# Performance work log

Measured on AMD Instinct MI355X. Metric: run time of the kernel, lower is better.

Reference implementation:

```python
import jax, jax.numpy as jnp
import numpy as np

HEAD_DIM = 32
N_HEADS = 8
Q_DIM = 128
FF_DIM = 4 * Q_DIM
EPS = 1e-5


def layernorm(x, gamma, beta):
    mu = jnp.mean(x, axis=-1, keepdims=True)
    var = jnp.var(x, axis=-1, keepdims=True)
    return (x - mu) * jax.lax.rsqrt(var + EPS) * gamma + beta


def setup_inputs() -> dict:
    key = jax.random.key(0)
    ks = jax.random.split(key, 20)
    S, B = 1024, 16
    sc_in = 1.0 / np.sqrt(Q_DIM)
    sc_hd = 1.0 / np.sqrt(N_HEADS * HEAD_DIM)
    sc_ff = 1.0 / np.sqrt(FF_DIM)
    return {
        "sequence": jax.random.normal(ks[0], (S, B, Q_DIM), jnp.float32),
        # per-head Q/K/V projections, stacked over heads: [H, Q_dim, head_dim]
        "Wq": jax.random.uniform(ks[1], (N_HEADS, Q_DIM, HEAD_DIM), jnp.float32, -sc_in, sc_in),
        "bq": jax.random.uniform(ks[2], (N_HEADS, HEAD_DIM), jnp.float32, -sc_in, sc_in),
        "Wk": jax.random.uniform(ks[3], (N_HEADS, Q_DIM, HEAD_DIM), jnp.float32, -sc_in, sc_in),
        "bk": jax.random.uniform(ks[4], (N_HEADS, HEAD_DIM), jnp.float32, -sc_in, sc_in),
        "Wv": jax.random.uniform(ks[5], (N_HEADS, Q_DIM, HEAD_DIM), jnp.float32, -sc_in, sc_in),
        "bv": jax.random.uniform(ks[6], (N_HEADS, HEAD_DIM), jnp.float32, -sc_in, sc_in),
        # post_head_linear: [H*head_dim, Q_dim]
        "Wo": jax.random.uniform(ks[7], (N_HEADS * HEAD_DIM, Q_DIM), jnp.float32, -sc_hd, sc_hd),
        "bo": jax.random.uniform(ks[8], (Q_DIM,), jnp.float32, -sc_hd, sc_hd),
        # norm1 (note: original reuses norm1 for both layernorms)
        "gamma1": jnp.ones((Q_DIM,), jnp.float32),
        "beta1": jnp.zeros((Q_DIM,), jnp.float32),
        # FFN: Q_dim -> 4Q -> 4Q -> Q_dim
        "W1": jax.random.uniform(ks[9], (Q_DIM, FF_DIM), jnp.float32, -sc_in, sc_in),
        "b1": jax.random.uniform(ks[10], (FF_DIM,), jnp.float32, -sc_in, sc_in),
        "W2": jax.random.uniform(ks[11], (FF_DIM, FF_DIM), jnp.float32, -sc_ff, sc_ff),
        "b2": jax.random.uniform(ks[12], (FF_DIM,), jnp.float32, -sc_ff, sc_ff),
        "W3": jax.random.uniform(ks[13], (FF_DIM, Q_DIM), jnp.float32, -sc_ff, sc_ff),
        "b3": jax.random.uniform(ks[14], (Q_DIM,), jnp.float32, -sc_ff, sc_ff),
    }


def reference(sequence, Wq, bq, Wk, bk, Wv, bv, Wo, bo, gamma1, beta1, W1, b1, W2, b2, W3, b3):
    # sequence: [S, B, Q_dim] -> batch-first [B, S, Q_dim]
    x = jnp.transpose(sequence, (1, 0, 2))
    # batched per-head projections: [B, H, S, d]
    q = jnp.einsum('bsq,hqd->bhsd', x, Wq) + bq[None, :, None, :]
    k = jnp.einsum('bsq,hqd->bhsd', x, Wk) + bk[None, :, None, :]
    v = jnp.einsum('bsq,hqd->bhsd', x, Wv) + bv[None, :, None, :]
    scores = jnp.einsum('bhsd,bhtd->bhst', q, k) / np.sqrt(HEAD_DIM)
    attn = jax.nn.softmax(scores, axis=-1)
    o = jnp.einsum('bhst,bhtd->bhsd', attn, v)  # [B, H, S, d]
    B, H, S, d = o.shape
    o = jnp.transpose(o, (0, 2, 1, 3)).reshape(B, S, H * d)  # concat heads
    att_outs = o @ Wo + bo
    att_outs = layernorm(x + att_outs, gamma1, beta1)
    h = jax.nn.relu(att_outs @ W1 + b1)
    h = jax.nn.relu(h @ W2 + b2)
    h = h @ W3 + b3
    out = layernorm(att_outs + h, gamma1, beta1)  # original reuses norm1
    return jnp.transpose(out, (1, 0, 2))  # back to [S, B, Q_dim]
```

## Files before the change

### kernel.cpp

```cpp
#include <hip/hip_runtime.h>
#include <hip/hip_bf16.h>

#define S_LEN 1024
#define BATCH 16
#define QD 128
#define NH 8
#define HD 32
#define FF 512
#define NROWS (BATCH * S_LEN)
#define EPS 1e-5f

typedef __attribute__((ext_vector_type(4))) float f32x4;
typedef __attribute__((ext_vector_type(8))) short s16x8;
typedef __attribute__((ext_vector_type(4))) short s16x4;

__device__ __forceinline__ ushort f2bfu(float f) {
    union { float f; unsigned u; } v; v.f = f;
    unsigned r = (v.u + 0x7FFFu + ((v.u >> 16) & 1u)) >> 16;
    return (ushort)r;
}

__device__ __forceinline__ float exp2_fast(float x) {
#if __has_builtin(__builtin_amdgcn_exp2f)
    return __builtin_amdgcn_exp2f(x);
#else
    float r;
    asm("v_exp_f32 %0, %1" : "=v"(r) : "v"(x));
    return r;
#endif
}

__device__ __forceinline__ unsigned pk_bf16(float a, float b) {
    union { __hip_bfloat162 h; unsigned u; } c;
    c.h = __float22bfloat162_rn(make_float2(a, b));
    return c.u;
}

static __device__ __forceinline__ f32x4 mfma16(s16x4 a, s16x4 b, f32x4 c) {
#if __has_builtin(__builtin_amdgcn_mfma_f32_16x16x16bf16_1k)
    return __builtin_amdgcn_mfma_f32_16x16x16bf16_1k(a, b, c, 0, 0, 0);
#else
    asm volatile("v_mfma_f32_16x16x16_bf16 %0, %1, %2, %0" : "+v"(c) : "v"(a), "v"(b));
    return c;
#endif
}

static __device__ __forceinline__ f32x4 mfma32(s16x8 a, s16x8 b, f32x4 c) {
    return __builtin_amdgcn_mfma_f32_16x16x32_bf16(a, b, c, 0, 0, 0);
}

__device__ __forceinline__ void gl_lds16(const void* g, void* l) {
    __builtin_amdgcn_global_load_lds(
        (const __attribute__((address_space(1))) void*)g,
        (__attribute__((address_space(3))) void*)l, 16, 0, 0);
}

template <int K>
__device__ __forceinline__ void gemm_core(
    const ushort* __restrict__ act, const ushort* __restrict__ WTp,
    char* lds, int tok0, f32x4 acc[8]) {
    const int tid = threadIdx.x;
    const int w = tid >> 6, lane = tid & 63;
    const int qi = lane & 15, g = lane >> 4;
    const int r8 = tid >> 3;
    const int csw = (tid & 7) ^ (r8 & 7);
    const int wave_base = w * 1024;
    constexpr int NT = K / 64;

    auto STAGE = [&](int b, int ks) {
        char* buf = lds + b * 24576;
#pragma unroll
        for (int i = 0; i < 4; ++i)
            gl_lds16(WTp + (size_t)(i * 32 + r8) * K + ks + csw * 8,
                     buf + i * 4096 + wave_base);
#pragma unroll
        for (int j = 0; j < 2; ++j)
            gl_lds16(act + (size_t)(tok0 + j * 32 + r8) * K + ks + csw * 8,
                     buf + 16384 + j * 4096 + wave_base);
    };

    STAGE(0, 0);
    int cur = 0;
#pragma unroll 1
    for (int t = 0; t < NT; ++t) {
        if (t < NT - 1) {
            STAGE(cur ^ 1, (t + 1) * 64);
            asm volatile("s_waitcnt vmcnt(6)" ::: "memory");
        } else {
            asm volatile("s_waitcnt vmcnt(0)" ::: "memory");
        }
        __builtin_amdgcn_sched_barrier(0);
        __builtin_amdgcn_s_barrier();
        __builtin_amdgcn_sched_barrier(0);
        const char* A = lds + cur * 24576;
        const char* B = A + 16384;
        const int brow = w * 16 + qi;
        __builtin_amdgcn_s_setprio(1);
#pragma unroll
        for (int kk2 = 0; kk2 < 2; ++kk2) {
            s16x8 bfrag = *(const s16x8*)(B + brow * 128 +
                                          (((kk2 * 4 + g) ^ (brow & 7)) * 16));
#pragma unroll
            for (int f = 0; f < 8; ++f) {
                const int row = qi + 16 * f;
                s16x8 afrag = *(const s16x8*)(A + row * 128 +
                                              (((kk2 * 4 + g) ^ (row & 7)) * 16));
                acc[f] = mfma32(afrag, bfrag, acc[f]);
            }
        }
        __builtin_amdgcn_s_setprio(0);
        __builtin_amdgcn_sched_barrier(0);
        __builtin_amdgcn_s_barrier();
        __builtin_amdgcn_sched_barrier(0);
        cur ^= 1;
    }
}

__global__ __launch_bounds__(256) void prep_weights(
    const float* __restrict__ Wo, const float* __restrict__ W1,
    const float* __restrict__ W2, const float* __restrict__ W3,
    const float* __restrict__ Wq, const float* __restrict__ Wk,
    const float* __restrict__ Wv,
    ushort* __restrict__ WoT, ushort* __restrict__ W1T,
    ushort* __restrict__ W2T, ushort* __restrict__ W3T,
    ushort* __restrict__ WqkvT) {
    int idx = blockIdx.x * 256 + threadIdx.x;
    if (idx < 32768) {
        int n = idx >> 8, k = idx & 255;
        WoT[n * 256 + k] = f2bfu(Wo[k * 128 + n]);
    } else if (idx < 98304) {
        int i = idx - 32768; int n = i >> 7, k = i & 127;
        W1T[n * 128 + k] = f2bfu(W1[k * 512 + n]);
    } else if (idx < 360448) {
        int i = idx - 98304; int n = i >> 9, k = i & 511;
        W2T[n * 512 + k] = f2bfu(W2[k * 512 + n]);
    } else if (idx < 425984) {
        int i = idx - 360448; int n = i >> 9, k = i & 511;
        W3T[n * 512 + k] = f2bfu(W3[k * 128 + n]);
    } else {
        int i = idx - 425984;
        int n = i >> 7, k = i & 127;
        int p = n >> 8, h = (n >> 5) & 7, d = n & 31;
        const float* W = (p == 0) ? Wq : (p == 1) ? Wk : Wv;
        WqkvT[n * 128 + k] = f2bfu(W[(h * QD + k) * HD + d]);
    }
}

__global__ __launch_bounds__(256) void seq2bf(
    const float* __restrict__ seq, ushort* __restrict__ x_bf) {
    int t = blockIdx.x * 256 + threadIdx.x;
    int e4 = t * 4;
    int s = e4 >> 11, b = (e4 >> 7) & 15, c = e4 & 127;
    float4 v = *(const float4*)(seq + e4);
    ushort4 o = {f2bfu(v.x), f2bfu(v.y), f2bfu(v.z), f2bfu(v.w)};
    *(ushort4*)(x_bf + ((size_t)(b * 1024 + s)) * 128 + c) = o;
}

__global__ __launch_bounds__(256) void qkv_mfma(
    const ushort* __restrict__ x_bf, const ushort* __restrict__ WqkvT,
    const float* __restrict__ bq, const float* __restrict__ bk,
    const float* __restrict__ bv,
    ushort* __restrict__ q_bf, ushort* __restrict__ k_bf,
    ushort* __restrict__ vT) {
    __shared__ __align__(16) char lds[2 * 24576];
    const int lane = threadIdx.x & 63;
    const int w = threadIdx.x >> 6;
    const int qi = lane & 15, g = lane >> 4;
    const int tok0 = blockIdx.x * 64;
    const int tok = tok0 + w * 16 + qi;
    const int n0 = blockIdx.y * 128;

    f32x4 acc[8];
#pragma unroll
    for (int f = 0; f < 8; ++f) acc[f] = (f32x4){0.f, 0.f, 0.f, 0.f};
    gemm_core<128>(x_bf, WqkvT + (size_t)n0 * 128, lds, tok0, acc);

    const int b = tok >> 10, s = tok & 1023;
    const float SCALE = 0.25503491f;
    if (n0 < 256) {
#pragma unroll
        for (int f = 0; f < 8; ++f)
#pragma unroll
            for (int r = 0; r < 4; ++r) {
                int n = n0 + 16 * f + 4 * g + r;
                int h = (n >> 5) & 7, d = n & 31;
                q_bf[((size_t)(b * 8 + h) * 1024 + s) * 32 + d] =
                    f2bfu((acc[f][r] + bq[h * 32 + d]) * SCALE);
            }
    } else if (n0 < 512) {
#pragma unroll
        for (int f = 0; f < 8; ++f)
#pragma unroll
            for (int r = 0; r < 4; ++r) {
                int n = n0 + 16 * f + 4 * g + r;
                int h = (n >> 5) & 7, d = n & 31;
                k_bf[((size_t)(b * 8 + h) * 1024 + s) * 32 + d] =
                    f2bfu(acc[f][r] + bk[h * 32 + d]);
            }
    } else {
#pragma unroll
        for (int f = 0; f < 8; ++f)
#pragma unroll
            for (int r = 0; r < 4; ++r) {
                int n = n0 + 16 * f + 4 * g + r;
                int h = (n >> 5) & 7, d = n & 31;
                vT[((size_t)(b * 8 + h) * 32 + d) * 1024 + s] =
                    f2bfu(acc[f][r] + bv[h * 32 + d]);
            }
    }
}

__global__ __launch_bounds__(256) void attn_mfma(
    const ushort* __restrict__ qb, const ushort* __restrict__ kb,
    const ushort* __restrict__ vtb, ushort* __restrict__ o_bf) {
    __shared__ __align__(16) char lds[2][8192];
    const int tid = threadIdx.x;
    const int w = tid >> 6, lane = tid & 63;
    const int g = lane >> 4, qi = lane & 15;
    const int bid = blockIdx.x;
    const int swz = (bid & 7) * 256 + (bid >> 3);
    const int bh = swz >> 4;
    const int qtile = (swz & 15) * 4 + w;

    const ushort* Kb = kb + (size_t)bh * S_LEN * HD;
    const ushort* VTb = vtb + (size_t)bh * HD * S_LEN;
    const s16x8 qf = *(const s16x8*)(qb + ((size_t)bh * S_LEN + qtile * 16 + qi) * HD + g * 8);

    const int krow = tid >> 2;
    const int ksw = (tid & 3) ^ ((tid >> 3) & 3);
    const int vrow = tid >> 3;
    const int vsw = (tid & 7) ^ ((tid >> 4) & 7);
    const int wave_off = w * 1024;

#define STAGE(bufp, k0)                                                          \
    do {                                                                         \
        gl_lds16(Kb + (size_t)((k0) + krow) * HD + ksw * 8, (bufp) + wave_off);  \
        gl_lds16(VTb + (size_t)vrow * S_LEN + (k0) + vsw * 8,                    \
                 (bufp) + 4096 + wave_off);                                      \
    } while (0)

    f32x4 ot0 = {0.f, 0.f, 0.f, 0.f};
    f32x4 ot1 = {0.f, 0.f, 0.f, 0.f};
    float m_run = -1e30f, l_run = 0.f;
    const f32x4 zero = {0.f, 0.f, 0.f, 0.f};

    const int koff = (g ^ ((qi >> 1) & 3)) * 16;
    const int vs = (qi >> 1) & 7;

    STAGE(lds[0], 0);
    int cur = 0;
#pragma unroll 1
    for (int t = 0; t < 16; ++t) {
        if (t < 15) {
            STAGE(lds[cur ^ 1], (t + 1) * 64);
            asm volatile("s_waitcnt vmcnt(2)" ::: "memory");
        } else {
            asm volatile("s_waitcnt vmcnt(0)" ::: "memory");
        }
        __builtin_amdgcn_sched_barrier(0);
        __builtin_amdgcn_s_barrier();
        __builtin_amdgcn_sched_barrier(0);

        const char* kl = lds[cur];
        const char* vl = lds[cur] + 4096;
        s16x8 ka[4];
#pragma unroll
        for (int kt = 0; kt < 4; ++kt)
            ka[kt] = *(const s16x8*)(kl + (16 * kt + qi) * 64 + koff);
        s16x4 va[2][4];
#pragma unroll
        for (int h = 0; h < 2; ++h)
#pragma unroll
            for (int kt = 0; kt < 4; ++kt) {
                int c8 = 4 * kt + g;
                va[h][kt] = *(const s16x4*)(vl + (16 * h + qi) * 128 +
                                            (((c8 >> 1) ^ vs) * 16) + (c8 & 1) * 8);
            }

        f32x4 st[4];
        __builtin_amdgcn_s_setprio(1);
#pragma unroll
        for (int kt = 0; kt < 4; ++kt) st[kt] = mfma32(ka[kt], qf, zero);
        __builtin_amdgcn_s_setprio(0);

        float a0 = fmaxf(fmaxf(st[0][0], st[0][1]), fmaxf(st[0][2], st[0][3]));
        float a1 = fmaxf(fmaxf(st[1][0], st[1][1]), fmaxf(st[1][2], st[1][3]));
        float a2 = fmaxf(fmaxf(st[2][0], st[2][1]), fmaxf(st[2][2], st[2][3]));
        float a3 = fmaxf(fmaxf(st[3][0], st[3][1]), fmaxf(st[3][2], st[3][3]));
        float pmax = fmaxf(fmaxf(a0, a1), fmaxf(a2, a3));

        if (!__all(pmax <= m_run + 8.0f)) {
            float mt = pmax;
            mt = fmaxf(mt, __shfl_xor(mt, 16, 64));
            mt = fmaxf(mt, __shfl_xor(mt, 32, 64));
            float m_new = fmaxf(m_run, mt);
            float alpha = exp2_fast(m_run - m_new);
            l_run *= alpha;
#pragma unroll
            for (int r = 0; r < 4; ++r) { ot0[r] *= alpha; ot1[r] *= alpha; }
            m_run = m_new;
        }

        float p[4][4];
#pragma unroll
        for (int kt = 0; kt < 4; ++kt)
#pragma unroll
            for (int r = 0; r < 4; ++r) p[kt][r] = exp2_fast(st[kt][r] - m_run);
        float s0 = (p[0][0] + p[0][1]) + (p[0][2] + p[0][3]);
        float s1 = (p[1][0] + p[1][1]) + (p[1][2] + p[1][3]);
        float s2 = (p[2][0] + p[2][1]) + (p[2][2] + p[2][3]);
        float s3 = (p[3][0] + p[3][1]) + (p[3][2] + p[3][3]);
        l_run += (s0 + s1) + (s2 + s3);

        union { s16x4 v; uint2 u; } pb[4];
#pragma unroll
        for (int kt = 0; kt < 4; ++kt) {
            pb[kt].u.x = pk_bf16(p[kt][0], p[kt][1]);
            pb[kt].u.y = pk_bf16(p[kt][2], p[kt][3]);
        }
        __builtin_amdgcn_s_setprio(1);
#pragma unroll
        for (int kt = 0; kt < 4; ++kt) {
            ot0 = mfma16(va[0][kt], pb[kt].v, ot0);
            ot1 = mfma16(va[1][kt], pb[kt].v, ot1);
        }
        __builtin_amdgcn_s_setprio(0);

        __builtin_amdgcn_sched_barrier(0);
        __builtin_amdgcn_s_barrier();
        __builtin_amdgcn_sched_barrier(0);
        cur ^= 1;
    }
#undef STAGE

    l_run += __shfl_xor(l_run, 16, 64);
    l_run += __shfl_xor(l_run, 32, 64);
    const float inv_l = 1.0f / l_run;
    const int b = bh >> 3, head = bh & 7;
    const int qg = qtile * 16 + qi;
    ushort* orow = o_bf + ((size_t)(b * S_LEN + qg)) * (NH * HD) + head * HD;
    ushort4 ob0 = {f2bfu(ot0[0] * inv_l), f2bfu(ot0[1] * inv_l),
                   f2bfu(ot0[2] * inv_l), f2bfu(ot0[3] * inv_l)};
    ushort4 ob1 = {f2bfu(ot1[0] * inv_l), f2bfu(ot1[1] * inv_l),
                   f2bfu(ot1[2] * inv_l), f2bfu(ot1[3] * inv_l)};
    *(ushort4*)(orow + g * 4) = ob0;
    *(ushort4*)(orow + 16 + g * 4) = ob1;
}

__global__ __launch_bounds__(256) void wo_ln_mfma(
    const ushort* __restrict__ o_bf, const ushort* __restrict__ WoT,
    const float* __restrict__ bo, const float* __restrict__ seq,
    const float* __restrict__ gamma, const float* __restrict__ beta,
    float* __restrict__ att, ushort* __restrict__ att_bf) {
    __shared__ __align__(16) char lds[2 * 24576];
    const int lane = threadIdx.x & 63;
    const int w = threadIdx.x >> 6;
    const int qi = lane & 15, g = lane >> 4;
    const int tok0 = blockIdx.x * 64;
    const int tok = tok0 + w * 16 + qi;

    f32x4 acc[8];
#pragma unroll
    for (int f = 0; f < 8; ++f) acc[f] = (f32x4){0.f, 0.f, 0.f, 0.f};
    gemm_core<256>(o_bf, WoT, lds, tok0, acc);

    const int b = tok >> 10, s = tok & 1023;
    const float* xrow = seq + (size_t)(s * BATCH + b) * QD;
    float sum = 0.f, sumsq = 0.f;
#pragma unroll
    for (int f = 0; f < 8; ++f) {
        const int c = 16 * f + 4 * g;
        float4 bv = *(const float4*)(bo + c);
        float4 xv = *(const float4*)(xrow + c);
        acc[f][0] += bv.x + xv.x;
        acc[f][1] += bv.y + xv.y;
        acc[f][2] += bv.z + xv.z;
        acc[f][3] += bv.w + xv.w;
#pragma unroll
        for (int r = 0; r < 4; ++r) { sum += acc[f][r]; sumsq += acc[f][r] * acc[f][r]; }
    }
    sum += __shfl_xor(sum, 16, 64);
    sum += __shfl_xor(sum, 32, 64);
    sumsq += __shfl_xor(sumsq, 16, 64);
    sumsq += __shfl_xor(sumsq, 32, 64);
    const float mu = sum * (1.0f / QD);
    const float var = sumsq * (1.0f / QD) - mu * mu;
    const float rstd = rsqrtf(var + EPS);

#pragma unroll
    for (int f = 0; f < 8; ++f) {
        const int c = 16 * f + 4 * g;
        float4 gm = *(const float4*)(gamma + c);
        float4 bt = *(const float4*)(beta + c);
        float4 ov;
        ov.x = (acc[f][0] - mu) * rstd * gm.x + bt.x;
        ov.y = (acc[f][1] - mu) * rstd * gm.y + bt.y;
        ov.z = (acc[f][2] - mu) * rstd * gm.z + bt.z;
        ov.w = (acc[f][3] - mu) * rstd * gm.w + bt.w;
        *(float4*)(att + (size_t)tok * QD + c) = ov;
        ushort4 pv = {f2bfu(ov.x), f2bfu(ov.y), f2bfu(ov.z), f2bfu(ov.w)};
        *(ushort4*)(att_bf + (size_t)tok * QD + c) = pv;
    }
}

template <int K>
__global__ __launch_bounds__(256) void ffn_mfma(
    const ushort* __restrict__ act, const ushort* __restrict__ WT,
    const float* __restrict__ bias, ushort* __restrict__ out, int N) {
    __shared__ __align__(16) char lds[2 * 24576];
    const int lane = threadIdx.x & 63;
    const int w = threadIdx.x >> 6;
    const int qi = lane & 15, g = lane >> 4;
    const int tok0 = blockIdx.x * 64;
    const int tok = tok0 + w * 16 + qi;
    const int n0 = blockIdx.y * 128;

    f32x4 acc[8];
#pragma unroll
    for (int f = 0; f < 8; ++f) acc[f] = (f32x4){0.f, 0.f, 0.f, 0.f};
    gemm_core<K>(act, WT + (size_t)n0 * K, lds, tok0, acc);

#pragma unroll
    for (int f = 0; f < 8; ++f) {
        const int c = n0 + 16 * f + 4 * g;
        float4 bv = *(const float4*)(bias + c);
        ushort4 pv;
        pv.x = f2bfu(fmaxf(acc[f][0] + bv.x, 0.f));
        pv.y = f2bfu(fmaxf(acc[f][1] + bv.y, 0.f));
        pv.z = f2bfu(fmaxf(acc[f][2] + bv.z, 0.f));
        pv.w = f2bfu(fmaxf(acc[f][3] + bv.w, 0.f));
        *(ushort4*)(out + (size_t)tok * N + c) = pv;
    }
}

__global__ __launch_bounds__(256) void w3_ln_mfma(
    const ushort* __restrict__ h2, const ushort* __restrict__ W3T,
    const float* __restrict__ b3, const float* __restrict__ att,
    const float* __restrict__ gamma, const float* __restrict__ beta,
    float* __restrict__ out) {
    __shared__ __align__(16) char lds[2 * 24576];
    const int lane = threadIdx.x & 63;
    const int w = threadIdx.x >> 6;
    const int qi = lane & 15, g = lane >> 4;
    const int tok0 = blockIdx.x * 64;
    const int tok = tok0 + w * 16 + qi;

    f32x4 acc[8];
#pragma unroll
    for (int f = 0; f < 8; ++f) acc[f] = (f32x4){0.f, 0.f, 0.f, 0.f};
    gemm_core<512>(h2, W3T, lds, tok0, acc);

    float sum = 0.f, sumsq = 0.f;
#pragma unroll
    for (int f = 0; f < 8; ++f) {
        const int c = 16 * f + 4 * g;
        float4 bv = *(const float4*)(b3 + c);
        float4 xv = *(const float4*)(att + (size_t)tok * QD + c);
        acc[f][0] += bv.x + xv.x;
        acc[f][1] += bv.y + xv.y;
        acc[f][2] += bv.z + xv.z;
        acc[f][3] += bv.w + xv.w;
#pragma unroll
        for (int r = 0; r < 4; ++r) { sum += acc[f][r]; sumsq += acc[f][r] * acc[f][r]; }
    }
    sum += __shfl_xor(sum, 16, 64);
    sum += __shfl_xor(sum, 32, 64);
    sumsq += __shfl_xor(sumsq, 16, 64);
    sumsq += __shfl_xor(sumsq, 32, 64);
    const float mu = sum * (1.0f / QD);
    const float var = sumsq * (1.0f / QD) - mu * mu;
    const float rstd = rsqrtf(var + EPS);

    const int b = tok >> 10, s = tok & 1023;
    float* orow = out + (size_t)(s * BATCH + b) * QD;
#pragma unroll
    for (int f = 0; f < 8; ++f) {
        const int c = 16 * f + 4 * g;
        float4 gm = *(const float4*)(gamma + c);
        float4 bt = *(const float4*)(beta + c);
        float4 ov;
        ov.x = (acc[f][0] - mu) * rstd * gm.x + bt.x;
        ov.y = (acc[f][1] - mu) * rstd * gm.y + bt.y;
        ov.z = (acc[f][2] - mu) * rstd * gm.z + bt.z;
        ov.w = (acc[f][3] - mu) * rstd * gm.w + bt.w;
        *(float4*)(orow + c) = ov;
    }
}

extern "C" void kernel_launch(void* const* d_in, const int* in_sizes, int n_in,
                              void* d_out, int out_size, void* d_ws, size_t ws_size,
                              hipStream_t stream) {
    const float* seq = (const float*)d_in[0];
    const float* Wq = (const float*)d_in[1];
    const float* bq = (const float*)d_in[2];
    const float* Wk = (const float*)d_in[3];
    const float* bk = (const float*)d_in[4];
    const float* Wv = (const float*)d_in[5];
    const float* bv = (const float*)d_in[6];
    const float* Wo = (const float*)d_in[7];
    const float* bo = (const float*)d_in[8];
    const float* gamma = (const float*)d_in[9];
    const float* beta = (const float*)d_in[10];
    const float* W1 = (const float*)d_in[11];
    const float* b1 = (const float*)d_in[12];
    const float* W2 = (const float*)d_in[13];
    const float* b2 = (const float*)d_in[14];
    const float* W3 = (const float*)d_in[15];
    const float* b3 = (const float*)d_in[16];

    char* wsb = (char*)d_ws;
    ushort* q_bf  = (ushort*)(wsb);
    ushort* k_bf  = (ushort*)(wsb + (8ull << 20));
    ushort* vT    = (ushort*)(wsb + (16ull << 20));
    ushort* o_bf  = (ushort*)(wsb + (24ull << 20));
    float*  att   = (float*)(wsb + (32ull << 20));
    ushort* att_bf= (ushort*)(wsb + (40ull << 20));
    ushort* h1_bf = (ushort*)(wsb);
    ushort* h2_bf = (ushort*)(wsb + (16ull << 20));
    ushort* x_bf  = (ushort*)(wsb + (45ull << 20));
    ushort* WoT   = (ushort*)(wsb + (49ull << 20));
    ushort* W1T   = WoT + 32768;
    ushort* W2T   = W1T + 65536;
    ushort* W3T   = W2T + 262144;
    ushort* WqkvT = W3T + 65536;
    float* out = (float*)d_out;

    prep_weights<<<2048, 256, 0, stream>>>(Wo, W1, W2, W3, Wq, Wk, Wv,
                                           WoT, W1T, W2T, W3T, WqkvT);
    seq2bf<<<2048, 256, 0, stream>>>(seq, x_bf);
    qkv_mfma<<<dim3(NROWS / 64, 6), 256, 0, stream>>>(x_bf, WqkvT, bq, bk, bv,
                                                      q_bf, k_bf, vT);
    attn_mfma<<<(BATCH * NH) * 16, 256, 0, stream>>>(q_bf, k_bf, vT, o_bf);
    wo_ln_mfma<<<NROWS / 64, 256, 0, stream>>>(o_bf, WoT, bo, seq, gamma, beta, att, att_bf);
    ffn_mfma<QD><<<dim3(NROWS / 64, 4), 256, 0, stream>>>(att_bf, W1T, b1, h1_bf, FF);
    ffn_mfma<FF><<<dim3(NROWS / 64, 4), 256, 0, stream>>>(h1_bf, W2T, b2, h2_bf, FF);
    w3_ln_mfma<<<NROWS / 64, 256, 0, stream>>>(h2_bf, W3T, b3, att, gamma, beta, out);
}
```

Baseline: 116.6 us.

## Merge prep kernels, widen attention blocks to 8 waves, drop fp32 residual buffer

Folds the sequence-to-bf16 conversion into the weight prep kernel, removing one launch. The attention kernel now runs 512-thread blocks with 8 query tiles per block, so each K/V tile staged in LDS is shared by twice as many waves and each wave issues one load instead of two. The fp32 post-attention residual buffer is removed and the final layernorm reads the bf16 copy, cutting global traffic at some cost in residual precision.

```diff
diff --git a/kernel.cpp b/kernel.cpp
--- a/kernel.cpp
+++ b/kernel.cpp
@@ -18,6 +18,11 @@
     union { float f; unsigned u; } v; v.f = f;
     unsigned r = (v.u + 0x7FFFu + ((v.u >> 16) & 1u)) >> 16;
     return (ushort)r;
+}
+
+__device__ __forceinline__ float bf2f(ushort u) {
+    union { unsigned u; float f; } v; v.u = ((unsigned)u) << 16;
+    return v.f;
 }
 
 __device__ __forceinline__ float exp2_fast(float x) {
@@ -116,7 +121,8 @@
     }
 }
 
-__global__ __launch_bounds__(256) void prep_weights(
+__global__ __launch_bounds__(256) void prep_all(
+    const float* __restrict__ seq, ushort* __restrict__ x_bf,
     const float* __restrict__ Wo, const float* __restrict__ W1,
     const float* __restrict__ W2, const float* __restrict__ W3,
     const float* __restrict__ Wq, const float* __restrict__ Wk,
@@ -124,7 +130,16 @@
     ushort* __restrict__ WoT, ushort* __restrict__ W1T,
     ushort* __restrict__ W2T, ushort* __restrict__ W3T,
     ushort* __restrict__ WqkvT) {
-    int idx = blockIdx.x * 256 + threadIdx.x;
+    if (blockIdx.x < 2048) {
+        int t = blockIdx.x * 256 + threadIdx.x;
+        int e4 = t * 4;
+        int s = e4 >> 11, b = (e4 >> 7) & 15, c = e4 & 127;
+        float4 v = *(const float4*)(seq + e4);
+        ushort4 o = {f2bfu(v.x), f2bfu(v.y), f2bfu(v.z), f2bfu(v.w)};
+        *(ushort4*)(x_bf + ((size_t)(b * 1024 + s)) * 128 + c) = o;
+        return;
+    }
+    int idx = (blockIdx.x - 2048) * 256 + threadIdx.x;
     if (idx < 32768) {
         int n = idx >> 8, k = idx & 255;
         WoT[n * 256 + k] = f2bfu(Wo[k * 128 + n]);
@@ -146,16 +161,6 @@
     }
 }
 
-__global__ __launch_bounds__(256) void seq2bf(
-    const float* __restrict__ seq, ushort* __restrict__ x_bf) {
-    int t = blockIdx.x * 256 + threadIdx.x;
-    int e4 = t * 4;
-    int s = e4 >> 11, b = (e4 >> 7) & 15, c = e4 & 127;
-    float4 v = *(const float4*)(seq + e4);
-    ushort4 o = {f2bfu(v.x), f2bfu(v.y), f2bfu(v.z), f2bfu(v.w)};
-    *(ushort4*)(x_bf + ((size_t)(b * 1024 + s)) * 128 + c) = o;
-}
-
 __global__ __launch_bounds__(256) void qkv_mfma(
     const ushort* __restrict__ x_bf, const ushort* __restrict__ WqkvT,
     const float* __restrict__ bq, const float* __restrict__ bk,
@@ -210,7 +215,7 @@
     }
 }
 
-__global__ __launch_bounds__(256) void attn_mfma(
+__global__ __launch_bounds__(512) void attn_mfma(
     const ushort* __restrict__ qb, const ushort* __restrict__ kb,
     const ushort* __restrict__ vtb, ushort* __restrict__ o_bf) {
     __shared__ __align__(16) char lds[2][8192];
@@ -218,25 +223,28 @@
     const int w = tid >> 6, lane = tid & 63;
     const int g = lane >> 4, qi = lane & 15;
     const int bid = blockIdx.x;
-    const int swz = (bid & 7) * 256 + (bid >> 3);
-    const int bh = swz >> 4;
-    const int qtile = (swz & 15) * 4 + w;
+    const int swz = (bid & 7) * 128 + (bid >> 3);
+    const int bh = swz >> 3;
+    const int qtile = (swz & 7) * 8 + w;
 
     const ushort* Kb = kb + (size_t)bh * S_LEN * HD;
     const ushort* VTb = vtb + (size_t)bh * HD * S_LEN;
     const s16x8 qf = *(const s16x8*)(qb + ((size_t)bh * S_LEN + qtile * 16 + qi) * HD + g * 8);
 
-    const int krow = tid >> 2;
-    const int ksw = (tid & 3) ^ ((tid >> 3) & 3);
-    const int vrow = tid >> 3;
-    const int vsw = (tid & 7) ^ ((tid >> 4) & 7);
-    const int wave_off = w * 1024;
-
-#define STAGE(bufp, k0)                                                          \
-    do {                                                                         \
-        gl_lds16(Kb + (size_t)((k0) + krow) * HD + ksw * 8, (bufp) + wave_off);  \
-        gl_lds16(VTb + (size_t)vrow * S_LEN + (k0) + vsw * 8,                    \
-                 (bufp) + 4096 + wave_off);                                      \
+    const int krow = 16 * w + (lane >> 2);
+    const int ksrc = (lane & 3) ^ ((lane >> 3) & 3);
+    const int wv = w & 3;
+    const int vrow = 8 * wv + (lane >> 3);
+    const int vsrc = (lane & 7) ^ ((4 * wv + (lane >> 4)) & 7);
+
+#define STAGE(bufp, k0)                                                        \
+    do {                                                                       \
+        if (w < 4)                                                             \
+            gl_lds16(Kb + (size_t)((k0) + krow) * HD + ksrc * 8,               \
+                     (bufp) + w * 1024);                                       \
+        else                                                                   \
+            gl_lds16(VTb + (size_t)vrow * S_LEN + (k0) + vsrc * 8,             \
+                     (bufp) + 4096 + wv * 1024);                               \
     } while (0)
 
     f32x4 ot0 = {0.f, 0.f, 0.f, 0.f};
@@ -253,7 +261,7 @@
     for (int t = 0; t < 16; ++t) {
         if (t < 15) {
             STAGE(lds[cur ^ 1], (t + 1) * 64);
-            asm volatile("s_waitcnt vmcnt(2)" ::: "memory");
+            asm volatile("s_waitcnt vmcnt(1)" ::: "memory");
         } else {
             asm volatile("s_waitcnt vmcnt(0)" ::: "memory");
         }
@@ -351,7 +359,7 @@
     const ushort* __restrict__ o_bf, const ushort* __restrict__ WoT,
     const float* __restrict__ bo, const float* __restrict__ seq,
     const float* __restrict__ gamma, const float* __restrict__ beta,
-    float* __restrict__ att, ushort* __restrict__ att_bf) {
+    ushort* __restrict__ att_bf) {
     __shared__ __align__(16) char lds[2 * 24576];
     const int lane = threadIdx.x & 63;
     const int w = threadIdx.x >> 6;
@@ -392,13 +400,11 @@
         const int c = 16 * f + 4 * g;
         float4 gm = *(const float4*)(gamma + c);
         float4 bt = *(const float4*)(beta + c);
-        float4 ov;
-        ov.x = (acc[f][0] - mu) * rstd * gm.x + bt.x;
-        ov.y = (acc[f][1] - mu) * rstd * gm.y + bt.y;
-        ov.z = (acc[f][2] - mu) * rstd * gm.z + bt.z;
-        ov.w = (acc[f][3] - mu) * rstd * gm.w + bt.w;
-        *(float4*)(att + (size_t)tok * QD + c) = ov;
-        ushort4 pv = {f2bfu(ov.x), f2bfu(ov.y), f2bfu(ov.z), f2bfu(ov.w)};
+        ushort4 pv;
+        pv.x = f2bfu((acc[f][0] - mu) * rstd * gm.x + bt.x);
+        pv.y = f2bfu((acc[f][1] - mu) * rstd * gm.y + bt.y);
+        pv.z = f2bfu((acc[f][2] - mu) * rstd * gm.z + bt.z);
+        pv.w = f2bfu((acc[f][3] - mu) * rstd * gm.w + bt.w);
         *(ushort4*)(att_bf + (size_t)tok * QD + c) = pv;
     }
 }
@@ -435,7 +441,7 @@
 
 __global__ __launch_bounds__(256) void w3_ln_mfma(
     const ushort* __restrict__ h2, const ushort* __restrict__ W3T,
-    const float* __restrict__ b3, const float* __restrict__ att,
+    const float* __restrict__ b3, const ushort* __restrict__ att_bf,
     const float* __restrict__ gamma, const float* __restrict__ beta,
     float* __restrict__ out) {
     __shared__ __align__(16) char lds[2 * 24576];
@@ -455,11 +461,11 @@
     for (int f = 0; f < 8; ++f) {
         const int c = 16 * f + 4 * g;
         float4 bv = *(const float4*)(b3 + c);
-        float4 xv = *(const float4*)(att + (size_t)tok * QD + c);
-        acc[f][0] += bv.x + xv.x;
-        acc[f][1] += bv.y + xv.y;
-        acc[f][2] += bv.z + xv.z;
-        acc[f][3] += bv.w + xv.w;
+        ushort4 xv = *(const ushort4*)(att_bf + (size_t)tok * QD + c);
+        acc[f][0] += bv.x + bf2f(xv.x);
+        acc[f][1] += bv.y + bf2f(xv.y);
+        acc[f][2] += bv.z + bf2f(xv.z);
+        acc[f][3] += bv.w + bf2f(xv.w);
 #pragma unroll
         for (int r = 0; r < 4; ++r) { sum += acc[f][r]; sumsq += acc[f][r] * acc[f][r]; }
     }
@@ -513,7 +519,6 @@
     ushort* k_bf  = (ushort*)(wsb + (8ull << 20));
     ushort* vT    = (ushort*)(wsb + (16ull << 20));
     ushort* o_bf  = (ushort*)(wsb + (24ull << 20));
-    float*  att   = (float*)(wsb + (32ull << 20));
     ushort* att_bf= (ushort*)(wsb + (40ull << 20));
     ushort* h1_bf = (ushort*)(wsb);
     ushort* h2_bf = (ushort*)(wsb + (16ull << 20));
@@ -525,14 +530,13 @@
     ushort* WqkvT = W3T + 65536;
     float* out = (float*)d_out;
 
-    prep_weights<<<2048, 256, 0, stream>>>(Wo, W1, W2, W3, Wq, Wk, Wv,
-                                           WoT, W1T, W2T, W3T, WqkvT);
-    seq2bf<<<2048, 256, 0, stream>>>(seq, x_bf);
+    prep_all<<<4096, 256, 0, stream>>>(seq, x_bf, Wo, W1, W2, W3, Wq, Wk, Wv,
+                                       WoT, W1T, W2T, W3T, WqkvT);
     qkv_mfma<<<dim3(NROWS / 64, 6), 256, 0, stream>>>(x_bf, WqkvT, bq, bk, bv,
                                                       q_bf, k_bf, vT);
-    attn_mfma<<<(BATCH * NH) * 16, 256, 0, stream>>>(q_bf, k_bf, vT, o_bf);
-    wo_ln_mfma<<<NROWS / 64, 256, 0, stream>>>(o_bf, WoT, bo, seq, gamma, beta, att, att_bf);
+    attn_mfma<<<1024, 512, 0, stream>>>(q_bf, k_bf, vT, o_bf);
+    wo_ln_mfma<<<NROWS / 64, 256, 0, stream>>>(o_bf, WoT, bo, seq, gamma, beta, att_bf);
     ffn_mfma<QD><<<dim3(NROWS / 64, 4), 256, 0, stream>>>(att_bf, W1T, b1, h1_bf, FF);
     ffn_mfma<FF><<<dim3(NROWS / 64, 4), 256, 0, stream>>>(h1_bf, W2T, b2, h2_bf, FF);
-    w3_ln_mfma<<<NROWS / 64, 256, 0, stream>>>(h2_bf, W3T, b3, att, gamma, beta, out);
-}
+    w3_ln_mfma<<<NROWS / 64, 256, 0, stream>>>(h2_bf, W3T, b3, att_bf, gamma, beta, out);
+}
```

Measured after the change: 109.2 us. -6.4%, faster.
